# Kernel optimization log

Measured on AMD Instinct MI355X. Metric: run time of the kernel, lower is better.

## Reference

```python
import jax, jax.numpy as jnp
import numpy as np

FIELD_SIZE = 39
FEATURE_SIZE = 100000
EMB = 10
BATCH = 2048

# Faithful to the original loop bounds: i in [0, F-2), j in [i+1, F-2)
# i.e. pairs (i, j) with i < j <= FIELD_SIZE - 2 (the last field is skipped
# in the pairwise term due to the original code's range(field_size - 1)).
_pairs = [(i, j) for i in range(FIELD_SIZE - 1) for j in range(i + 1, FIELD_SIZE - 1)]
_I = np.array([p[0] for p in _pairs], dtype=np.int32)  # [P] = [703]
_J = np.array([p[1] for p in _pairs], dtype=np.int32)


def setup_inputs() -> dict:
    key = jax.random.key(0)
    k1, k2, k3, k4 = jax.random.split(key, 4)
    idxs = jax.random.randint(k1, (BATCH, FIELD_SIZE), 0, FEATURE_SIZE)
    vals = jax.random.uniform(k2, (BATCH, FIELD_SIZE), dtype=jnp.float32)
    # stacked field-aware embedding tables: emb_tables[f] == self.emb[f].weight
    emb_tables = jax.random.normal(k3, (FIELD_SIZE, FEATURE_SIZE, EMB), dtype=jnp.float32) * 0.01
    w1 = jax.random.normal(k4, (FEATURE_SIZE, 1), dtype=jnp.float32) * 0.01
    return {"idxs": idxs, "vals": vals, "emb_tables": emb_tables, "w1": w1}


def reference(idxs, vals, emb_tables, w1):
    # first order: sum_f w1[idxs[b,f]] * vals[b,f]
    first = jnp.sum(w1[idxs].squeeze(-1) * vals, axis=1)  # [B]

    i_idx = jnp.asarray(_I)  # [P]
    j_idx = jnp.asarray(_J)  # [P]
    # ffm_second_order_embs[i][:, j] == emb_tables[i, idxs[:, j]] * vals[:, j, None]
    # Only gather the (field, column) entries the pairwise loop actually uses.
    a = emb_tables[i_idx[None, :], idxs[:, j_idx]] * vals[:, j_idx, None]  # [B,P,E]
    b = emb_tables[j_idx[None, :], idxs[:, i_idx]] * vals[:, i_idx, None]  # [B,P,E]
    second = jnp.sum(a * b, axis=(1, 2))  # cat over pairs then sum dim=1 == sum over P and E

    return jax.nn.sigmoid(first + second)  # [B]
```

## Files before the change

### kernel.cpp

```cpp
#include <hip/hip_runtime.h>
#include <math.h>

#define FIELD  39
#define NPF    38
#define NPAIRS 703
#define FEAT   100000
#define EMB    10

#define CHUNK_B    464
#define CHUNK_U32  116
#define CHUNK_U16B 29
#define ROW_B      12
#define RCOLS      32

#define SCALE      512.0f
#define INV_SCALE2 3.814697265625e-06f

typedef float floatx2 __attribute__((ext_vector_type(2)));
typedef const void __attribute__((address_space(1)))* gas_ptr;
typedef void       __attribute__((address_space(3)))* las_ptr;

__device__ __forceinline__ void decode_pair(int p, int& i_out, int& j_out) {
    const float disc = 5625.0f - 8.0f * (float)p;
    int i = (int)((75.0f - sqrtf(disc)) * 0.5f);
    int off = (i * (75 - i)) >> 1;
    if (p < off) {
        --i; off = (i * (75 - i)) >> 1;
    } else {
        const int off1 = ((i + 1) * (74 - i)) >> 1;
        if (p >= off1) { ++i; off = off1; }
    }
    i_out = i;
    j_out = i + 1 + (p - off);
}

__global__ __launch_bounds__(256) void repack_kernel(
    const float4* __restrict__ emb4, uint4* __restrict__ T4)
{
    __shared__ unsigned char sB[RCOLS * CHUNK_B];
    const int t  = threadIdx.x;
    const int bx = blockIdx.x;
    const float4* __restrict__ base = emb4 + (size_t)80 * bx;

    #pragma unroll
    for (int g = 0; g < 2; ++g) {
        float4 v[6];
        int    ib[6], e0[6];
        bool   ok[6];
        #pragma unroll
        for (int k = 0; k < 6; ++k) {
            const int u = t + (6 * g + k) * 256;
            ok[k] = (u < NPF * 80);
            const int uc = ok[k] ? u : 0;
            const int i  = (int)(((unsigned)uc * 52429u) >> 22);
            const int q  = uc - i * 80;
            ib[k] = i;
            e0[k] = q << 2;
            v[k]  = base[i * 250000 + q];
        }
        #pragma unroll
        for (int k = 0; k < 6; ++k) {
            if (!ok[k]) continue;
            const unsigned lo = __builtin_amdgcn_cvt_pk_fp8_f32(v[k].x * SCALE, v[k].y * SCALE, 0, false);
            const unsigned hi = __builtin_amdgcn_cvt_pk_fp8_f32(v[k].z * SCALE, v[k].w * SCALE, 0, false);
            const int i = ib[k];
            {
                const int e   = e0[k];
                const int col = (e * 6554) >> 16;
                const int off = e - 10 * col;
                *(ushort*)(sB + col * CHUNK_B + i * ROW_B + off) = (ushort)lo;
            }
            {
                const int e   = e0[k] + 2;
                const int col = (e * 6554) >> 16;
                const int off = e - 10 * col;
                *(ushort*)(sB + col * CHUNK_B + i * ROW_B + off) = (ushort)hi;
            }
        }
    }
    __syncthreads();

    const uint4* s4 = (const uint4*)sB;
    for (int u = t; u < RCOLS * CHUNK_U16B; u += 256)
        T4[(size_t)bx * (RCOLS * CHUNK_U16B) + u] = s4[u];
}

__global__ __launch_bounds__(256) void ffm_kernel(
    const int*   __restrict__ idxs,
    const float* __restrict__ vals,
    const uint4* __restrict__ T4,
    const float* __restrict__ w1,
    float*       __restrict__ out)
{
    const int b = blockIdx.x;
    const int t = threadIdx.x;

    __shared__ int      s_idx[FIELD];
    __shared__ float    s_val[FIELD];
    __shared__ unsigned sM[NPF * CHUNK_U32];

    if (t < FIELD) {
        s_idx[t] = idxs[b * FIELD + t];
        s_val[t] = vals[b * FIELD + t];
    }
    __syncthreads();

    float acc = (t < FIELD) ? w1[s_idx[t]] * s_val[t] : 0.f;

    {
        uint4* sM4 = (uint4*)sM;
        #pragma unroll
        for (int g = 0; g < 5; ++g) {
            const int u = t + g * 256;
            if (u < NPF * CHUNK_U16B) {
                const int f  = (u * 2261) >> 16;
                const int k4 = u - f * CHUNK_U16B;
                const uint4* src = T4 + (size_t)s_idx[f] * CHUNK_U16B + k4;
                __builtin_amdgcn_global_load_lds((gas_ptr)src, (las_ptr)(sM4 + u), 16, 0, 0);
            }
        }
    }
    __syncthreads();

    #pragma unroll
    for (int k = 0; k < 3; ++k) {
        int p = t + (k << 8);
        const bool valid = (p < NPAIRS);
        p = valid ? p : (NPAIRS - 1);
        int i, j;
        decode_pair(p, i, j);
        const float vv = s_val[i] * s_val[j] * INV_SCALE2;
        const unsigned* A = sM + j * CHUNK_U32 + 3 * i;
        const unsigned* B = sM + i * CHUNK_U32 + 3 * j;
        const unsigned a0 = A[0], a1 = A[1], a2 = A[2];
        const unsigned b0 = B[0], b1 = B[1], b2 = B[2];
        floatx2 s2;
        s2  = (floatx2)__builtin_amdgcn_cvt_pk_f32_fp8(a0, false) *
              (floatx2)__builtin_amdgcn_cvt_pk_f32_fp8(b0, false);
        s2 += (floatx2)__builtin_amdgcn_cvt_pk_f32_fp8(a0, true ) *
              (floatx2)__builtin_amdgcn_cvt_pk_f32_fp8(b0, true );
        s2 += (floatx2)__builtin_amdgcn_cvt_pk_f32_fp8(a1, false) *
              (floatx2)__builtin_amdgcn_cvt_pk_f32_fp8(b1, false);
        s2 += (floatx2)__builtin_amdgcn_cvt_pk_f32_fp8(a1, true ) *
              (floatx2)__builtin_amdgcn_cvt_pk_f32_fp8(b1, true );
        s2 += (floatx2)__builtin_amdgcn_cvt_pk_f32_fp8(a2, false) *
              (floatx2)__builtin_amdgcn_cvt_pk_f32_fp8(b2, false);
        const float s = s2.x + s2.y;
        acc += valid ? s * vv : 0.f;
    }

    #pragma unroll
    for (int off = 32; off > 0; off >>= 1)
        acc += __shfl_down(acc, off, 64);

    __shared__ float wsum[4];
    if ((t & 63) == 0) wsum[t >> 6] = acc;
    __syncthreads();
    if (t == 0) {
        const float tot = wsum[0] + wsum[1] + wsum[2] + wsum[3];
        out[b] = 1.f / (1.f + expf(-tot));
    }
}

extern "C" void kernel_launch(void* const* d_in, const int* in_sizes, int n_in,
                              void* d_out, int out_size, void* d_ws, size_t ws_size,
                              hipStream_t stream) {
    const int*   idxs = (const int*)  d_in[0];
    const float* vals = (const float*)d_in[1];
    const float* emb  = (const float*)d_in[2];
    const float* w1   = (const float*)d_in[3];
    float*       out  = (float*)d_out;
    uint4*       T4   = (uint4*)d_ws;

    repack_kernel<<<FEAT / RCOLS, 256, 0, stream>>>((const float4*)emb, T4);
    ffm_kernel<<<out_size, 256, 0, stream>>>(idxs, vals, T4, w1, out);
}
```

Baseline: 241.7 us.

## Skip repacking embedding columns for features not referenced by the batch

A new kernel marks every feature index used by the batch by writing a zero flag into workspace memory. The repack kernel then loads, converts and stores only the table columns whose flag is zero, so it reads less of the large embedding table. Flags are never reset to nonzero, so any skipping depends on the workspace starting with nonzero bytes. Stale zero flags only cause extra work, not wrong results. The change also adds an extra kernel launch and a shared-memory flag lookup.

```diff
diff --git a/kernel.cpp b/kernel.cpp
--- a/kernel.cpp
+++ b/kernel.cpp
@@ -15,6 +15,8 @@
 
 #define SCALE      512.0f
 #define INV_SCALE2 3.814697265625e-06f
+
+#define FLAGS_OFF  (48u * 1024u * 1024u)
 
 typedef float floatx2 __attribute__((ext_vector_type(2)));
 typedef const void __attribute__((address_space(1)))* gas_ptr;
@@ -34,13 +36,28 @@
     j_out = i + 1 + (p - off);
 }
 
+__global__ __launch_bounds__(256) void flag_kernel(
+    const int* __restrict__ idxs, unsigned char* __restrict__ flags, int nref)
+{
+    const int g = blockIdx.x * 256 + threadIdx.x;
+    if (g >= nref) return;
+    const int b = (int)(((unsigned long long)g * 220753ull) >> 23);
+    const int f = g - b * NPF;
+    flags[idxs[b * FIELD + f]] = 0;
+}
+
 __global__ __launch_bounds__(256) void repack_kernel(
-    const float4* __restrict__ emb4, uint4* __restrict__ T4)
+    const float4* __restrict__ emb4, uint4* __restrict__ T4,
+    const unsigned char* __restrict__ flags)
 {
     __shared__ unsigned char sB[RCOLS * CHUNK_B];
+    __shared__ unsigned char sFlag[RCOLS];
     const int t  = threadIdx.x;
     const int bx = blockIdx.x;
     const float4* __restrict__ base = emb4 + (size_t)80 * bx;
+
+    if (t < RCOLS) sFlag[t] = flags[bx * RCOLS + t];
+    __syncthreads();
 
     #pragma unroll
     for (int g = 0; g < 2; ++g) {
@@ -50,13 +67,16 @@
         #pragma unroll
         for (int k = 0; k < 6; ++k) {
             const int u = t + (6 * g + k) * 256;
-            ok[k] = (u < NPF * 80);
-            const int uc = ok[k] ? u : 0;
+            const bool inb = (u < NPF * 80);
+            const int uc = inb ? u : 0;
             const int i  = (int)(((unsigned)uc * 52429u) >> 22);
             const int q  = uc - i * 80;
             ib[k] = i;
             e0[k] = q << 2;
-            v[k]  = base[i * 250000 + q];
+            const int cA = (e0[k] * 6554) >> 16;
+            const int cB = ((e0[k] + 3) * 6554) >> 16;
+            ok[k] = inb && ((sFlag[cA] == 0) || (sFlag[cB] == 0));
+            v[k] = ok[k] ? base[i * 250000 + q] : float4{0.f, 0.f, 0.f, 0.f};
         }
         #pragma unroll
         for (int k = 0; k < 6; ++k) {
@@ -81,8 +101,11 @@
     __syncthreads();
 
     const uint4* s4 = (const uint4*)sB;
-    for (int u = t; u < RCOLS * CHUNK_U16B; u += 256)
-        T4[(size_t)bx * (RCOLS * CHUNK_U16B) + u] = s4[u];
+    for (int u = t; u < RCOLS * CHUNK_U16B; u += 256) {
+        const int col = (u * 2261) >> 16;
+        if (sFlag[col] == 0)
+            T4[(size_t)bx * (RCOLS * CHUNK_U16B) + u] = s4[u];
+    }
 }
 
 __global__ __launch_bounds__(256) void ffm_kernel(
@@ -171,7 +194,12 @@
     const float* w1   = (const float*)d_in[3];
     float*       out  = (float*)d_out;
     uint4*       T4   = (uint4*)d_ws;
-
-    repack_kernel<<<FEAT / RCOLS, 256, 0, stream>>>((const float4*)emb, T4);
-    ffm_kernel<<<out_size, 256, 0, stream>>>(idxs, vals, T4, w1, out);
-}
+    unsigned char* flags = (unsigned char*)d_ws + FLAGS_OFF;
+
+    const int B    = out_size;
+    const int nref = B * NPF;
+
+    flag_kernel<<<(nref + 255) / 256, 256, 0, stream>>>(idxs, flags, nref);
+    repack_kernel<<<FEAT / RCOLS, 256, 0, stream>>>((const float4*)emb, T4, flags);
+    ffm_kernel<<<B, 256, 0, stream>>>(idxs, vals, T4, w1, out);
+}
```

Measured after the change: 244.9 us. No clear change (+1.3%).

## Repack embeddings per column in registers and write directly without LDS staging

Applied to the files above, without the earlier changes.

The repack kernel now gives each thread one feature column and four fields. It converts those values to fp8 in registers and writes 48 bytes straight to the workspace, so the shared-memory staging buffer and block barrier are gone. The per-column chunk is padded from 464 to 480 bytes so every group of four fields fills exactly three 16-byte stores. The ffm kernel's chunk stride and division constant are updated to match. In exchange, the ffm kernel gathers slightly more bytes per row, and the global stores are strided by column, which may coalesce worse than the old contiguous copy-out.

```diff
diff --git a/kernel.cpp b/kernel.cpp
--- a/kernel.cpp
+++ b/kernel.cpp
@@ -7,10 +7,9 @@
 #define FEAT   100000
 #define EMB    10
 
-#define CHUNK_B    464
-#define CHUNK_U32  116
-#define CHUNK_U16B 29
-#define ROW_B      12
+#define CHUNK_B    480
+#define CHUNK_U32  120
+#define CHUNK_U16B 30
 #define RCOLS      32
 
 #define SCALE      512.0f
@@ -34,55 +33,45 @@
     j_out = i + 1 + (p - off);
 }
 
-__global__ __launch_bounds__(256) void repack_kernel(
-    const float4* __restrict__ emb4, uint4* __restrict__ T4)
+__global__ __launch_bounds__(320) void repack_kernel(
+    const float2* __restrict__ emb2, uint4* __restrict__ T4)
 {
-    __shared__ unsigned char sB[RCOLS * CHUNK_B];
-    const int t  = threadIdx.x;
-    const int bx = blockIdx.x;
-    const float4* __restrict__ base = emb4 + (size_t)80 * bx;
+    const int t   = threadIdx.x;
+    const int c   = t & 31;
+    const int g   = t >> 5;
+    const int col = blockIdx.x * RCOLS + c;
 
+    float2 v[4][5];
     #pragma unroll
-    for (int g = 0; g < 2; ++g) {
-        float4 v[6];
-        int    ib[6], e0[6];
-        bool   ok[6];
+    for (int r = 0; r < 4; ++r) {
+        const int  i    = 4 * g + r;
+        const bool real = (i < NPF);
+        const float2* src = emb2 + (size_t)(real ? i : 0) * 500000 + col * 5;
         #pragma unroll
-        for (int k = 0; k < 6; ++k) {
-            const int u = t + (6 * g + k) * 256;
-            ok[k] = (u < NPF * 80);
-            const int uc = ok[k] ? u : 0;
-            const int i  = (int)(((unsigned)uc * 52429u) >> 22);
-            const int q  = uc - i * 80;
-            ib[k] = i;
-            e0[k] = q << 2;
-            v[k]  = base[i * 250000 + q];
-        }
-        #pragma unroll
-        for (int k = 0; k < 6; ++k) {
-            if (!ok[k]) continue;
-            const unsigned lo = __builtin_amdgcn_cvt_pk_fp8_f32(v[k].x * SCALE, v[k].y * SCALE, 0, false);
-            const unsigned hi = __builtin_amdgcn_cvt_pk_fp8_f32(v[k].z * SCALE, v[k].w * SCALE, 0, false);
-            const int i = ib[k];
-            {
-                const int e   = e0[k];
-                const int col = (e * 6554) >> 16;
-                const int off = e - 10 * col;
-                *(ushort*)(sB + col * CHUNK_B + i * ROW_B + off) = (ushort)lo;
-            }
-            {
-                const int e   = e0[k] + 2;
-                const int col = (e * 6554) >> 16;
-                const int off = e - 10 * col;
-                *(ushort*)(sB + col * CHUNK_B + i * ROW_B + off) = (ushort)hi;
-            }
+        for (int k = 0; k < 5; ++k) {
+            const float2 x = src[k];
+            v[r][k].x = real ? x.x : 0.f;
+            v[r][k].y = real ? x.y : 0.f;
         }
     }
-    __syncthreads();
 
-    const uint4* s4 = (const uint4*)sB;
-    for (int u = t; u < RCOLS * CHUNK_U16B; u += 256)
-        T4[(size_t)bx * (RCOLS * CHUNK_U16B) + u] = s4[u];
+    unsigned dw[12];
+    #pragma unroll
+    for (int r = 0; r < 4; ++r) {
+        unsigned d0 = __builtin_amdgcn_cvt_pk_fp8_f32(v[r][0].x * SCALE, v[r][0].y * SCALE, 0, false);
+        d0 = __builtin_amdgcn_cvt_pk_fp8_f32(v[r][1].x * SCALE, v[r][1].y * SCALE, d0, true);
+        unsigned d1 = __builtin_amdgcn_cvt_pk_fp8_f32(v[r][2].x * SCALE, v[r][2].y * SCALE, 0, false);
+        d1 = __builtin_amdgcn_cvt_pk_fp8_f32(v[r][3].x * SCALE, v[r][3].y * SCALE, d1, true);
+        const unsigned d2 = __builtin_amdgcn_cvt_pk_fp8_f32(v[r][4].x * SCALE, v[r][4].y * SCALE, 0, false);
+        dw[3 * r]     = d0;
+        dw[3 * r + 1] = d1;
+        dw[3 * r + 2] = d2;
+    }
+
+    uint4* dst = T4 + (size_t)col * CHUNK_U16B + 3 * g;
+    dst[0] = uint4{dw[0], dw[1], dw[2],  dw[3]};
+    dst[1] = uint4{dw[4], dw[5], dw[6],  dw[7]};
+    dst[2] = uint4{dw[8], dw[9], dw[10], dw[11]};
 }
 
 __global__ __launch_bounds__(256) void ffm_kernel(
@@ -113,7 +102,7 @@
         for (int g = 0; g < 5; ++g) {
             const int u = t + g * 256;
             if (u < NPF * CHUNK_U16B) {
-                const int f  = (u * 2261) >> 16;
+                const int f  = (u * 2185) >> 16;
                 const int k4 = u - f * CHUNK_U16B;
                 const uint4* src = T4 + (size_t)s_idx[f] * CHUNK_U16B + k4;
                 __builtin_amdgcn_global_load_lds((gas_ptr)src, (las_ptr)(sM4 + u), 16, 0, 0);
@@ -172,6 +161,6 @@
     float*       out  = (float*)d_out;
     uint4*       T4   = (uint4*)d_ws;
 
-    repack_kernel<<<FEAT / RCOLS, 256, 0, stream>>>((const float4*)emb, T4);
+    repack_kernel<<<FEAT / RCOLS, 320, 0, stream>>>((const float2*)emb, T4);
     ffm_kernel<<<out_size, 256, 0, stream>>>(idxs, vals, T4, w1, out);
 }
```

Measured after the change: 251.6 us. +4.1%, slower.
